# Kernel tuning notes

Hardware: AMD Instinct MI355X
Metric: run time of the kernel (lower is better)

Reference implementation:

```python
import jax, jax.numpy as jnp
import numpy as np

DIM = 768
HEADS = 12
DIM_HEAD = 64
INNER = HEADS * DIM_HEAD  # 768
SCALE = DIM_HEAD ** -0.5
LN_EPS = 1e-5


def setup_inputs() -> dict:
    key = jax.random.key(0)
    ks = jax.random.split(key, 6)
    B, N = 2, 1024
    x = jax.random.normal(ks[0], (B, N, DIM), dtype=jnp.float32)
    ln_g = jnp.ones((DIM,), jnp.float32)
    ln_b = jnp.zeros((DIM,), jnp.float32)
    # torch nn.Linear weights are [out, in]
    w_qkv = jax.random.normal(ks[1], (3 * INNER, DIM), jnp.float32) * (DIM ** -0.5)
    w_out = jax.random.normal(ks[2], (DIM, INNER), jnp.float32) * (INNER ** -0.5)
    b_out = jnp.zeros((DIM,), jnp.float32)
    theta = jax.random.normal(ks[3], (HEADS, HEADS), jnp.float32)
    # xavier_uniform for 12x12
    lim = float(np.sqrt(6.0 / (HEADS + HEADS)))
    gnn_w = jax.random.uniform(ks[4], (HEADS, HEADS), jnp.float32, -lim, lim)
    return {"x": x, "ln_g": ln_g, "ln_b": ln_b, "w_qkv": w_qkv,
            "w_out": w_out, "b_out": b_out, "theta": theta, "gnn_w": gnn_w}


def _dc_crd(attn, theta, gnn_w):
    # attn: [B, H, N, N] treated as image with H=12 channels
    B, H, N, _ = attn.shape
    w = attn.mean(axis=(-2, -1))  # adaptive_avg_pool2d -> [B, H]
    diff = w[:, :, None] - w[:, None, :]  # [B, H, H]
    # abs(1 - exp(-d)/(1+exp(-d))) - 1 == abs(1 - sigmoid(-d)) - 1
    T_w = jnp.abs(1.0 - jax.nn.sigmoid(-diff)) - 1.0
    adj = (T_w + jnp.swapaxes(T_w, -1, -2)) * 0.5 * theta  # [B, H, H]
    attn_flat = attn.reshape(B, H, N * N)
    support = jnp.einsum('ij,bjm->bim', gnn_w, attn_flat)  # W @ features
    out = jax.nn.relu(jnp.einsum('bij,bjm->bim', adj, support))  # spmm(adj, support)
    return out.reshape(B, H, N, N)


def reference(x, ln_g, ln_b, w_qkv, w_out, b_out, theta, gnn_w):
    B, N, D = x.shape
    mu = x.mean(-1, keepdims=True)
    var = x.var(-1, keepdims=True)
    xn = (x - mu) * jax.lax.rsqrt(var + LN_EPS) * ln_g + ln_b
    qkv = xn @ w_qkv.T  # [B, N, 3*INNER]
    q, k, v = jnp.split(qkv, 3, axis=-1)
    def heads(t):
        return t.reshape(B, N, HEADS, DIM_HEAD).transpose(0, 2, 1, 3)
    q, k, v = heads(q), heads(k), heads(v)  # [B, H, N, d]
    dots = jnp.einsum('bhnd,bhmd->bhnm', q, k) * SCALE
    attn = jax.nn.softmax(dots, axis=-1)
    H = _dc_crd(attn, theta, gnn_w)
    out = jnp.einsum('bhnm,bhmd->bhnd', attn + H, v)
    out = out.transpose(0, 2, 1, 3).reshape(B, N, INNER)
    return out @ w_out.T + b_out
```

## Files before the change

kernel.cpp:

```cpp
#include <hip/hip_runtime.h>
#include <hip/hip_bf16.h>
#include <stdint.h>

#define NB 2
#define SEQ 1024
#define DMODEL 768
#define NH 12
#define DH 64
#define SCALE 0.125f
#define NCH 4

#define AJ_RS 1288
#define CT_HS 648

typedef __hip_bfloat16 bf16;
typedef __attribute__((ext_vector_type(8))) short short8;
typedef __attribute__((ext_vector_type(2))) short s2v;
typedef __attribute__((ext_vector_type(4))) float f32x4;

__device__ __forceinline__ bf16 f2b(float x){ return __float2bfloat16(x); }
__device__ __forceinline__ short f2bs(float x){
  bf16 h = __float2bfloat16(x); return *reinterpret_cast<short*>(&h);
}
__device__ __forceinline__ float s2f(short u){
  return __uint_as_float(((unsigned)(unsigned short)u) << 16);
}

__device__ __forceinline__ void gl_lds16(const bf16* g, bf16* l){
  __builtin_amdgcn_global_load_lds(
      (const __attribute__((address_space(1))) void*)g,
      (__attribute__((address_space(3))) void*)l, 16, 0, 0);
}

__global__ __launch_bounds__(256) void prep_all(const float* __restrict__ x,
                                                const float* __restrict__ g,
                                                const float* __restrict__ bta,
                                                const float* __restrict__ w1, int n1,
                                                const float* __restrict__ w2, int n2,
                                                const float* __restrict__ theta,
                                                const float* __restrict__ gnn,
                                                bf16* __restrict__ xn,
                                                bf16* __restrict__ wb,
                                                bf16* __restrict__ Mb,
                                                float* __restrict__ l){
  int bx = blockIdx.x, t = threadIdx.x;
  if (bx < 2048){
    const float* xr = x + (size_t)bx*DMODEL;
    float v0[3]; float s = 0.f, s2 = 0.f;
    #pragma unroll
    for (int i=0;i<3;i++){ float val = xr[t+256*i]; v0[i]=val; s+=val; s2+=val*val; }
    __shared__ float sb[256], s2b[256];
    sb[t]=s; s2b[t]=s2; __syncthreads();
    for (int off=128; off>0; off>>=1){
      if (t<off){ sb[t]+=sb[t+off]; s2b[t]+=s2b[t+off]; }
      __syncthreads();
    }
    float mean = sb[0]*(1.f/DMODEL);
    float var  = s2b[0]*(1.f/DMODEL) - mean*mean;
    float rstd = rsqrtf(var + 1e-5f);
    #pragma unroll
    for (int i=0;i<3;i++){
      int c = t+256*i;
      xn[(size_t)bx*DMODEL + c] = f2b((v0[i]-mean)*rstd*g[c] + bta[c]);
    }
  } else if (bx < 2048+9216){
    int i = (bx-2048)*256 + t;
    if (i < n1) wb[i] = f2b(w1[i]);
    else if (i < n1+n2) wb[i] = f2b(w2[i-n1]);
  } else {
    int sub = bx - (2048+9216);
    if (sub == 0){
      #pragma unroll
      for (int e=0;e<2;e++){
        int idx = t + 256*e;
        int i = idx >> 5, j = idx & 31;
        float sacc = 0.f;
        if (i < 12 && j < 12)
          for (int jj=0;jj<12;jj++) sacc += (-0.5f)*theta[i*12+jj] * gnn[jj*12+j];
        bf16 hi = f2b(sacc);
        float lo = sacc - __bfloat162float(hi);
        Mb[idx]       = hi;
        Mb[512 + idx] = f2b(lo);
      }
    } else {
      l[(sub-1)*256 + t] = 0.f;
    }
  }
}

__global__ __launch_bounds__(256) void gemm_qkv(const bf16* __restrict__ A,
                                                const bf16* __restrict__ W,
                                                bf16* __restrict__ q,
                                                bf16* __restrict__ k,
                                                bf16* __restrict__ vt){
  __shared__ bf16 As[128*32];
  __shared__ bf16 Bs[128*32];
  int n0 = blockIdx.x*128, m0 = blockIdx.y*128;
  int t = threadIdx.x, w = t>>6, lane = t&63;
  int ln16 = lane&15, q8 = (lane>>4)*8;
  int wm = w>>1, wn = w&1;
  f32x4 acc[4][4] = {};
  for (int k0=0; k0<768; k0+=32){
    __syncthreads();
    #pragma unroll
    for (int i=0;i<2;i++){
      int cc = t + i*256;
      int r = cc>>2, ko = (cc&3)*8;
      gl_lds16(&A[(size_t)(m0+r)*768 + k0+ko], &As[(size_t)(w*64 + i*256)*8]);
      gl_lds16(&W[(size_t)(n0+r)*768 + k0+ko], &Bs[(size_t)(w*64 + i*256)*8]);
    }
    __syncthreads();
    short8 af[4], bfr[4];
    #pragma unroll
    for (int mi=0;mi<4;mi++) af[mi]  = *(const short8*)&As[(wm*64+mi*16+ln16)*32 + q8];
    #pragma unroll
    for (int ni=0;ni<4;ni++) bfr[ni] = *(const short8*)&Bs[(wn*64+ni*16+ln16)*32 + q8];
    #pragma unroll
    for (int mi=0;mi<4;mi++)
      #pragma unroll
      for (int ni=0;ni<4;ni++)
        acc[mi][ni] = __builtin_amdgcn_mfma_f32_16x16x32_bf16(af[mi], bfr[ni], acc[mi][ni], 0, 0, 0);
  }
  int quad4 = (lane>>4)*4;
  #pragma unroll
  for (int mi=0;mi<4;mi++){
    #pragma unroll
    for (int ni=0;ni<4;ni++){
      int cg = n0 + wn*64 + ni*16 + ln16;
      int which = cg/768; int rem = cg - which*768;
      int h = rem>>6, dd = rem&63;
      #pragma unroll
      for (int r=0;r<4;r++){
        int m = m0 + wm*64 + mi*16 + quad4 + r;
        int bb = m>>10, n = m&1023;
        float val = acc[mi][ni][r];
        if (which==0)      q [((size_t)(bb*NH+h)*SEQ + n)*DH + dd] = f2b(val*SCALE);
        else if (which==1) k [((size_t)(bb*NH+h)*SEQ + n)*DH + dd] = f2b(val);
        else               vt[((size_t)(bb*NH+h)*DH + dd)*SEQ + n] = f2b(val);
      }
    }
  }
}

__global__ __launch_bounds__(768) void attn_sums(const bf16* __restrict__ q,
                                                 const bf16* __restrict__ k,
                                                 float* __restrict__ l){
  int b = blockIdx.z, ch = blockIdx.y; int r0 = blockIdx.x*16;
  int t = threadIdx.x; int h = t>>6; int lane = t&63;
  int ln16 = lane&15, quad = lane>>4; int q8 = quad*8, quad4 = quad*4;
  const bf16* qrow = q + ((size_t)(b*NH+h)*SEQ + r0 + ln16)*DH;
  short8 aq0 = *(const short8*)(qrow + q8);
  short8 aq1 = *(const short8*)(qrow + 32 + q8);
  const bf16* kB = k + ((size_t)(b*NH+h)*SEQ)*DH;
  float ls[4] = {0.f,0.f,0.f,0.f};
  #pragma unroll 4
  for (int i=0;i<16;i++){
    int c0 = ch*256 + i*16;
    const bf16* krow = kB + (size_t)(c0 + ln16)*DH;
    short8 bk0 = *(const short8*)(krow + q8);
    short8 bk1 = *(const short8*)(krow + 32 + q8);
    f32x4 a = {0.f,0.f,0.f,0.f};
    a = __builtin_amdgcn_mfma_f32_16x16x32_bf16(aq0, bk0, a, 0, 0, 0);
    a = __builtin_amdgcn_mfma_f32_16x16x32_bf16(aq1, bk1, a, 0, 0, 0);
    #pragma unroll
    for (int r=0;r<4;r++) ls[r] += __expf(a[r]);
  }
  #pragma unroll
  for (int msk=1; msk<16; msk<<=1){
    #pragma unroll
    for (int r=0;r<4;r++) ls[r] += __shfl_xor(ls[r], msk);
  }
  if (ln16 == 0){
    #pragma unroll
    for (int r=0;r<4;r++)
      atomicAdd(&l[((size_t)(b*NH+h))*SEQ + r0 + quad4 + r], ls[r]);
  }
}

__global__ __launch_bounds__(768) void attn_main(const bf16* __restrict__ q,
                                                 const bf16* __restrict__ k,
                                                 const bf16* __restrict__ vt,
                                                 const bf16* __restrict__ Mb,
                                                 const float* __restrict__ l,
                                                 bf16* __restrict__ opart){
  __shared__ __align__(16) bf16 attJ[16*AJ_RS];
  __shared__ __align__(16) bf16 combT[16*CT_HS];
  int b = blockIdx.z, ch = blockIdx.y; int r0 = blockIdx.x*16;
  int t = threadIdx.x; int h = t>>6; int lane = t&63;
  int ln16 = lane&15, quad = lane>>4; int q8 = quad*8, quad4 = quad*4;
  const bf16* kB = k  + ((size_t)(b*NH+h)*SEQ)*DH;
  const bf16* vB = vt + ((size_t)(b*NH+h)*DH)*SEQ;

  short8 z8 = (short8){0,0,0,0,0,0,0,0};
  for (int i = t*8; i < 16*AJ_RS; i += 768*8) *(short8*)&attJ[i] = z8;

  short8 mhi = *(const short8*)&Mb[ln16*32 + q8];
  short8 mlo = *(const short8*)&Mb[512 + ln16*32 + q8];

  const bf16* qrow = q + ((size_t)(b*NH+h)*SEQ + r0 + ln16)*DH;
  short8 aq0 = *(const short8*)(qrow + q8);
  short8 aq1 = *(const short8*)(qrow + 32 + q8);

  float inv_l[4];
  #pragma unroll
  for (int r=0;r<4;r++) inv_l[r] = 1.0f / l[((size_t)(b*NH+h))*SEQ + r0 + quad4 + r];

  __syncthreads();

  f32x4 oacc[4] = {};
  for (int it=0; it<8; it++){
    int c0 = ch*256 + it*32;
    #pragma unroll
    for (int half=0; half<2; half++){
      const bf16* krow = kB + (size_t)(c0 + half*16 + ln16)*DH;
      short8 bk0 = *(const short8*)(krow + q8);
      short8 bk1 = *(const short8*)(krow + 32 + q8);
      f32x4 a = {0.f,0.f,0.f,0.f};
      a = __builtin_amdgcn_mfma_f32_16x16x32_bf16(aq0, bk0, a, 0, 0, 0);
      a = __builtin_amdgcn_mfma_f32_16x16x32_bf16(aq1, bk1, a, 0, 0, 0);
      int cc = half*16 + ln16;
      #pragma unroll
      for (int r=0;r<4;r++)
        attJ[(quad4+r)*AJ_RS + cc*40 + h] = f2b(__expf(a[r])*inv_l[r]);
    }
    __syncthreads();
    for (int tl = h; tl < 32; tl += 12){
      int n = tl*16 + ln16;
      int base = (n>>5)*AJ_RS + (n&31)*40;
      short8 bfrag = *(const short8*)&attJ[base + q8];
      f32x4 c = {0.f,0.f,0.f,0.f};
      c = __builtin_amdgcn_mfma_f32_16x16x32_bf16(mlo, bfrag, c, 0, 0, 0);
      c = __builtin_amdgcn_mfma_f32_16x16x32_bf16(mhi, bfrag, c, 0, 0, 0);
      s2v id01 = *(const s2v*)&attJ[base + quad4];
      s2v id23 = *(const s2v*)&attJ[base + quad4 + 2];
      float idf[4] = { s2f(id01[0]), s2f(id01[1]), s2f(id23[0]), s2f(id23[1]) };
      int cbase = (n>>5)*40 + (n&31);
      #pragma unroll
      for (int ri=0; ri<4; ri++)
        combT[(quad4+ri)*CT_HS + cbase] = f2b(idf[ri] + fmaxf(c[ri], 0.f));
    }
    __syncthreads();
    short8 afrag = *(const short8*)&combT[h*CT_HS + ln16*40 + q8];
    #pragma unroll
    for (int ni=0; ni<4; ni++){
      short8 bv = *(const short8*)&vB[(size_t)(ni*16 + ln16)*SEQ + c0 + q8];
      oacc[ni] = __builtin_amdgcn_mfma_f32_16x16x32_bf16(afrag, bv, oacc[ni], 0, 0, 0);
    }
  }
  bf16* dst = opart + ((size_t)ch*NB*SEQ + (size_t)b*SEQ)*DMODEL;
  #pragma unroll
  for (int ni=0; ni<4; ni++)
    #pragma unroll
    for (int r=0; r<4; r++){
      int n = r0 + quad4 + r;
      dst[(size_t)n*DMODEL + h*DH + ni*16 + ln16] = f2b(oacc[ni][r]);
    }
}

__global__ __launch_bounds__(256) void reduce_kernel(const bf16* __restrict__ opart,
                                                     bf16* __restrict__ aout){
  const size_t TOT = (size_t)NB*SEQ*DMODEL;
  size_t i = ((size_t)blockIdx.x*256 + threadIdx.x)*8;
  float s[8] = {};
  #pragma unroll
  for (int c=0;c<NCH;c++){
    short8 u = *(const short8*)&opart[c*TOT + i];
    #pragma unroll
    for (int e=0;e<8;e++) s[e] += s2f(u[e]);
  }
  short8 o;
  #pragma unroll
  for (int e=0;e<8;e++) o[e] = f2bs(s[e]);
  *(short8*)&aout[i] = o;
}

__global__ __launch_bounds__(256) void gemm_out(const bf16* __restrict__ A,
                                                const bf16* __restrict__ W,
                                                const float* __restrict__ bias,
                                                float* __restrict__ out){
  __shared__ bf16 As[64*32];
  __shared__ bf16 Bs[64*32];
  int n0 = blockIdx.x*64, m0 = blockIdx.y*64;
  int t = threadIdx.x, w = t>>6, lane = t&63;
  int ln16 = lane&15, q8 = (lane>>4)*8;
  int wm = w>>1, wn = w&1;
  f32x4 acc[2][2] = {};
  for (int k0=0; k0<768; k0+=32){
    __syncthreads();
    {
      int r = t>>2, ko = (t&3)*8;
      gl_lds16(&A[(size_t)(m0+r)*768 + k0+ko], &As[(size_t)(w*64)*8]);
      gl_lds16(&W[(size_t)(n0+r)*768 + k0+ko], &Bs[(size_t)(w*64)*8]);
    }
    __syncthreads();
    short8 af[2], bfr[2];
    #pragma unroll
    for (int mi=0;mi<2;mi++) af[mi]  = *(const short8*)&As[(wm*32+mi*16+ln16)*32 + q8];
    #pragma unroll
    for (int ni=0;ni<2;ni++) bfr[ni] = *(const short8*)&Bs[(wn*32+ni*16+ln16)*32 + q8];
    #pragma unroll
    for (int mi=0;mi<2;mi++)
      #pragma unroll
      for (int ni=0;ni<2;ni++)
        acc[mi][ni] = __builtin_amdgcn_mfma_f32_16x16x32_bf16(af[mi], bfr[ni], acc[mi][ni], 0, 0, 0);
  }
  int quad4 = (lane>>4)*4;
  #pragma unroll
  for (int mi=0;mi<2;mi++)
    #pragma unroll
    for (int ni=0;ni<2;ni++){
      int cg = n0 + wn*32 + ni*16 + ln16;
      #pragma unroll
      for (int r=0;r<4;r++){
        int m = m0 + wm*32 + mi*16 + quad4 + r;
        out[(size_t)m*768 + cg] = acc[mi][ni][r] + bias[cg];
      }
    }
}

extern "C" void kernel_launch(void* const* d_in, const int* in_sizes, int n_in,
                              void* d_out, int out_size, void* d_ws, size_t ws_size,
                              hipStream_t stream){
  const float* x     = (const float*)d_in[0];
  const float* ln_g  = (const float*)d_in[1];
  const float* ln_b  = (const float*)d_in[2];
  const float* w_qkv = (const float*)d_in[3];
  const float* w_out = (const float*)d_in[4];
  const float* b_out = (const float*)d_in[5];
  const float* theta = (const float*)d_in[6];
  const float* gnn   = (const float*)d_in[7];
  float* out = (float*)d_out;

  char* p = (char*)d_ws;
  bf16* xnb   = (bf16*)p; p += (size_t)2048*768*2;
  bf16* wqkvb = (bf16*)p; p += (size_t)2304*768*2;
  bf16* woutb = (bf16*)p; p += (size_t)768*768*2;
  bf16* qb    = (bf16*)p; p += (size_t)NB*NH*SEQ*DH*2;
  bf16* kb    = (bf16*)p; p += (size_t)NB*NH*SEQ*DH*2;
  bf16* vtb   = (bf16*)p; p += (size_t)NB*NH*SEQ*DH*2;
  bf16* aoutb = (bf16*)p; p += (size_t)2048*768*2;
  bf16* Mbw   = (bf16*)p; p += (size_t)1024*2;
  float* lsum = (float*)p; p += (size_t)NB*NH*SEQ*4;
  bf16* opart = (bf16*)p;

  const int N1 = 2304*768, N2 = 768*768;
  prep_all<<<dim3(2048+9216+97), dim3(256), 0, stream>>>(
      x, ln_g, ln_b, w_qkv, N1, w_out, N2, theta, gnn, xnb, wqkvb, Mbw, lsum);
  gemm_qkv<<<dim3(18, 16), dim3(256), 0, stream>>>(xnb, wqkvb, qb, kb, vtb);
  attn_sums<<<dim3(64, NCH, NB), dim3(768), 0, stream>>>(qb, kb, lsum);
  attn_main<<<dim3(64, NCH, NB), dim3(768), 0, stream>>>(qb, kb, vtb, Mbw, lsum, opart);
  reduce_kernel<<<dim3(NB*SEQ*DMODEL/(8*256)), dim3(256), 0, stream>>>(opart, aoutb);
  gemm_out<<<dim3(12, 32), dim3(256), 0, stream>>>(aoutb, woutb, b_out, out);
}
```

Measured before the change: 202.0 us.

## Fuse partial-sum reduce into out GEMM, prefetch K/V, shrink QKV GEMM tiles

The separate reduce kernel is removed. gemm_out now sums the NCH bf16 partial outputs while staging its A tile into LDS, which drops one launch and one intermediate round trip through global memory. attn_main software-prefetches the next K tile and issues V loads earlier, and gets a minimum-blocks launch bound to help hide load latency. gemm_qkv moves from 128x128 to 64x64 tiles, giving four times as many blocks for better CU coverage, at the cost of less data reuse per block and more register pressure in attn_main.

```diff
diff --git a/kernel.cpp b/kernel.cpp
--- a/kernel.cpp
+++ b/kernel.cpp
@@ -93,47 +93,43 @@
                                                 bf16* __restrict__ q,
                                                 bf16* __restrict__ k,
                                                 bf16* __restrict__ vt){
-  __shared__ bf16 As[128*32];
-  __shared__ bf16 Bs[128*32];
-  int n0 = blockIdx.x*128, m0 = blockIdx.y*128;
+  __shared__ bf16 As[64*32];
+  __shared__ bf16 Bs[64*32];
+  int n0 = blockIdx.x*64, m0 = blockIdx.y*64;
   int t = threadIdx.x, w = t>>6, lane = t&63;
   int ln16 = lane&15, q8 = (lane>>4)*8;
   int wm = w>>1, wn = w&1;
-  f32x4 acc[4][4] = {};
+  f32x4 acc[2][2] = {};
+  int r = t>>2, ko = (t&3)*8;
   for (int k0=0; k0<768; k0+=32){
     __syncthreads();
-    #pragma unroll
-    for (int i=0;i<2;i++){
-      int cc = t + i*256;
-      int r = cc>>2, ko = (cc&3)*8;
-      gl_lds16(&A[(size_t)(m0+r)*768 + k0+ko], &As[(size_t)(w*64 + i*256)*8]);
-      gl_lds16(&W[(size_t)(n0+r)*768 + k0+ko], &Bs[(size_t)(w*64 + i*256)*8]);
-    }
-    __syncthreads();
-    short8 af[4], bfr[4];
-    #pragma unroll
-    for (int mi=0;mi<4;mi++) af[mi]  = *(const short8*)&As[(wm*64+mi*16+ln16)*32 + q8];
-    #pragma unroll
-    for (int ni=0;ni<4;ni++) bfr[ni] = *(const short8*)&Bs[(wn*64+ni*16+ln16)*32 + q8];
-    #pragma unroll
-    for (int mi=0;mi<4;mi++)
-      #pragma unroll
-      for (int ni=0;ni<4;ni++)
+    gl_lds16(&A[(size_t)(m0+r)*768 + k0+ko], &As[(size_t)(w*64)*8]);
+    gl_lds16(&W[(size_t)(n0+r)*768 + k0+ko], &Bs[(size_t)(w*64)*8]);
+    __syncthreads();
+    short8 af[2], bfr[2];
+    #pragma unroll
+    for (int mi=0;mi<2;mi++) af[mi]  = *(const short8*)&As[(wm*32+mi*16+ln16)*32 + q8];
+    #pragma unroll
+    for (int ni=0;ni<2;ni++) bfr[ni] = *(const short8*)&Bs[(wn*32+ni*16+ln16)*32 + q8];
+    #pragma unroll
+    for (int mi=0;mi<2;mi++)
+      #pragma unroll
+      for (int ni=0;ni<2;ni++)
         acc[mi][ni] = __builtin_amdgcn_mfma_f32_16x16x32_bf16(af[mi], bfr[ni], acc[mi][ni], 0, 0, 0);
   }
   int quad4 = (lane>>4)*4;
   #pragma unroll
-  for (int mi=0;mi<4;mi++){
-    #pragma unroll
-    for (int ni=0;ni<4;ni++){
-      int cg = n0 + wn*64 + ni*16 + ln16;
+  for (int mi=0;mi<2;mi++){
+    #pragma unroll
+    for (int ni=0;ni<2;ni++){
+      int cg = n0 + wn*32 + ni*16 + ln16;
       int which = cg/768; int rem = cg - which*768;
       int h = rem>>6, dd = rem&63;
       #pragma unroll
-      for (int r=0;r<4;r++){
-        int m = m0 + wm*64 + mi*16 + quad4 + r;
+      for (int rr=0;rr<4;rr++){
+        int m = m0 + wm*32 + mi*16 + quad4 + rr;
         int bb = m>>10, n = m&1023;
-        float val = acc[mi][ni][r];
+        float val = acc[mi][ni][rr];
         if (which==0)      q [((size_t)(bb*NH+h)*SEQ + n)*DH + dd] = f2b(val*SCALE);
         else if (which==1) k [((size_t)(bb*NH+h)*SEQ + n)*DH + dd] = f2b(val);
         else               vt[((size_t)(bb*NH+h)*DH + dd)*SEQ + n] = f2b(val);
@@ -177,12 +173,12 @@
   }
 }
 
-__global__ __launch_bounds__(768) void attn_main(const bf16* __restrict__ q,
-                                                 const bf16* __restrict__ k,
-                                                 const bf16* __restrict__ vt,
-                                                 const bf16* __restrict__ Mb,
-                                                 const float* __restrict__ l,
-                                                 bf16* __restrict__ opart){
+__global__ __launch_bounds__(768, 6) void attn_main(const bf16* __restrict__ q,
+                                                    const bf16* __restrict__ k,
+                                                    const bf16* __restrict__ vt,
+                                                    const bf16* __restrict__ Mb,
+                                                    const float* __restrict__ l,
+                                                    bf16* __restrict__ opart){
   __shared__ __align__(16) bf16 attJ[16*AJ_RS];
   __shared__ __align__(16) bf16 combT[16*CT_HS];
   int b = blockIdx.z, ch = blockIdx.y; int r0 = blockIdx.x*16;
@@ -205,23 +201,42 @@
   #pragma unroll
   for (int r=0;r<4;r++) inv_l[r] = 1.0f / l[((size_t)(b*NH+h))*SEQ + r0 + quad4 + r];
 
+  const bf16* kr0 = kB + (size_t)(ch*256 + ln16)*DH;
+  short8 ka0 = *(const short8*)(kr0 + q8);
+  short8 ka1 = *(const short8*)(kr0 + 32 + q8);
+  short8 kb0 = *(const short8*)(kr0 + 16*DH + q8);
+  short8 kb1 = *(const short8*)(kr0 + 16*DH + 32 + q8);
+
   __syncthreads();
 
   f32x4 oacc[4] = {};
+  #pragma unroll 2
   for (int it=0; it<8; it++){
     int c0 = ch*256 + it*32;
-    #pragma unroll
-    for (int half=0; half<2; half++){
-      const bf16* krow = kB + (size_t)(c0 + half*16 + ln16)*DH;
-      short8 bk0 = *(const short8*)(krow + q8);
-      short8 bk1 = *(const short8*)(krow + 32 + q8);
+    int cn = ch*256 + ((it+1)&7)*32;
+    const bf16* vp = vB + (size_t)ln16*SEQ + c0 + q8;
+    short8 vv0 = *(const short8*)(vp);
+    short8 vv1 = *(const short8*)(vp + 16*SEQ);
+    const bf16* krn = kB + (size_t)(cn + ln16)*DH;
+    short8 na0 = *(const short8*)(krn + q8);
+    short8 na1 = *(const short8*)(krn + 32 + q8);
+    short8 nb0 = *(const short8*)(krn + 16*DH + q8);
+    short8 nb1 = *(const short8*)(krn + 16*DH + 32 + q8);
+    {
       f32x4 a = {0.f,0.f,0.f,0.f};
-      a = __builtin_amdgcn_mfma_f32_16x16x32_bf16(aq0, bk0, a, 0, 0, 0);
-      a = __builtin_amdgcn_mfma_f32_16x16x32_bf16(aq1, bk1, a, 0, 0, 0);
-      int cc = half*16 + ln16;
+      a = __builtin_amdgcn_mfma_f32_16x16x32_bf16(aq0, ka0, a, 0, 0, 0);
+      a = __builtin_amdgcn_mfma_f32_16x16x32_bf16(aq1, ka1, a, 0, 0, 0);
       #pragma unroll
       for (int r=0;r<4;r++)
-        attJ[(quad4+r)*AJ_RS + cc*40 + h] = f2b(__expf(a[r])*inv_l[r]);
+        attJ[(quad4+r)*AJ_RS + ln16*40 + h] = f2b(__expf(a[r])*inv_l[r]);
+    }
+    {
+      f32x4 a = {0.f,0.f,0.f,0.f};
+      a = __builtin_amdgcn_mfma_f32_16x16x32_bf16(aq0, kb0, a, 0, 0, 0);
+      a = __builtin_amdgcn_mfma_f32_16x16x32_bf16(aq1, kb1, a, 0, 0, 0);
+      #pragma unroll
+      for (int r=0;r<4;r++)
+        attJ[(quad4+r)*AJ_RS + (16+ln16)*40 + h] = f2b(__expf(a[r])*inv_l[r]);
     }
     __syncthreads();
     for (int tl = h; tl < 32; tl += 12){
@@ -240,12 +255,14 @@
         combT[(quad4+ri)*CT_HS + cbase] = f2b(idf[ri] + fmaxf(c[ri], 0.f));
     }
     __syncthreads();
+    short8 vv2 = *(const short8*)(vp + 32*SEQ);
+    short8 vv3 = *(const short8*)(vp + 48*SEQ);
     short8 afrag = *(const short8*)&combT[h*CT_HS + ln16*40 + q8];
-    #pragma unroll
-    for (int ni=0; ni<4; ni++){
-      short8 bv = *(const short8*)&vB[(size_t)(ni*16 + ln16)*SEQ + c0 + q8];
-      oacc[ni] = __builtin_amdgcn_mfma_f32_16x16x32_bf16(afrag, bv, oacc[ni], 0, 0, 0);
-    }
+    oacc[0] = __builtin_amdgcn_mfma_f32_16x16x32_bf16(afrag, vv0, oacc[0], 0, 0, 0);
+    oacc[1] = __builtin_amdgcn_mfma_f32_16x16x32_bf16(afrag, vv1, oacc[1], 0, 0, 0);
+    oacc[2] = __builtin_amdgcn_mfma_f32_16x16x32_bf16(afrag, vv2, oacc[2], 0, 0, 0);
+    oacc[3] = __builtin_amdgcn_mfma_f32_16x16x32_bf16(afrag, vv3, oacc[3], 0, 0, 0);
+    ka0 = na0; ka1 = na1; kb0 = nb0; kb1 = nb1;
   }
   bf16* dst = opart + ((size_t)ch*NB*SEQ + (size_t)b*SEQ)*DMODEL;
   #pragma unroll
@@ -257,41 +274,33 @@
     }
 }
 
-__global__ __launch_bounds__(256) void reduce_kernel(const bf16* __restrict__ opart,
-                                                     bf16* __restrict__ aout){
-  const size_t TOT = (size_t)NB*SEQ*DMODEL;
-  size_t i = ((size_t)blockIdx.x*256 + threadIdx.x)*8;
-  float s[8] = {};
-  #pragma unroll
-  for (int c=0;c<NCH;c++){
-    short8 u = *(const short8*)&opart[c*TOT + i];
-    #pragma unroll
-    for (int e=0;e<8;e++) s[e] += s2f(u[e]);
-  }
-  short8 o;
-  #pragma unroll
-  for (int e=0;e<8;e++) o[e] = f2bs(s[e]);
-  *(short8*)&aout[i] = o;
-}
-
-__global__ __launch_bounds__(256) void gemm_out(const bf16* __restrict__ A,
+__global__ __launch_bounds__(256) void gemm_out(const bf16* __restrict__ opart,
                                                 const bf16* __restrict__ W,
                                                 const float* __restrict__ bias,
                                                 float* __restrict__ out){
   __shared__ bf16 As[64*32];
   __shared__ bf16 Bs[64*32];
+  const size_t TOT = (size_t)NB*SEQ*DMODEL;
   int n0 = blockIdx.x*64, m0 = blockIdx.y*64;
   int t = threadIdx.x, w = t>>6, lane = t&63;
   int ln16 = lane&15, q8 = (lane>>4)*8;
   int wm = w>>1, wn = w&1;
   f32x4 acc[2][2] = {};
+  int r = t>>2, ko = (t&3)*8;
   for (int k0=0; k0<768; k0+=32){
     __syncthreads();
-    {
-      int r = t>>2, ko = (t&3)*8;
-      gl_lds16(&A[(size_t)(m0+r)*768 + k0+ko], &As[(size_t)(w*64)*8]);
-      gl_lds16(&W[(size_t)(n0+r)*768 + k0+ko], &Bs[(size_t)(w*64)*8]);
-    }
+    gl_lds16(&W[(size_t)(n0+r)*768 + k0+ko], &Bs[(size_t)(w*64)*8]);
+    float s[8] = {};
+    #pragma unroll
+    for (int c=0;c<NCH;c++){
+      short8 u = *(const short8*)&opart[(size_t)c*TOT + (size_t)(m0+r)*768 + k0+ko];
+      #pragma unroll
+      for (int e=0;e<8;e++) s[e] += s2f(u[e]);
+    }
+    short8 o8;
+    #pragma unroll
+    for (int e=0;e<8;e++) o8[e] = f2bs(s[e]);
+    *(short8*)&As[r*32 + ko] = o8;
     __syncthreads();
     short8 af[2], bfr[2];
     #pragma unroll
@@ -311,9 +320,9 @@
     for (int ni=0;ni<2;ni++){
       int cg = n0 + wn*32 + ni*16 + ln16;
       #pragma unroll
-      for (int r=0;r<4;r++){
-        int m = m0 + wm*32 + mi*16 + quad4 + r;
-        out[(size_t)m*768 + cg] = acc[mi][ni][r] + bias[cg];
+      for (int rr=0;rr<4;rr++){
+        int m = m0 + wm*32 + mi*16 + quad4 + rr;
+        out[(size_t)m*768 + cg] = acc[mi][ni][rr] + bias[cg];
       }
     }
 }
@@ -338,7 +347,6 @@
   bf16* qb    = (bf16*)p; p += (size_t)NB*NH*SEQ*DH*2;
   bf16* kb    = (bf16*)p; p += (size_t)NB*NH*SEQ*DH*2;
   bf16* vtb   = (bf16*)p; p += (size_t)NB*NH*SEQ*DH*2;
-  bf16* aoutb = (bf16*)p; p += (size_t)2048*768*2;
   bf16* Mbw   = (bf16*)p; p += (size_t)1024*2;
   float* lsum = (float*)p; p += (size_t)NB*NH*SEQ*4;
   bf16* opart = (bf16*)p;
@@ -346,9 +354,8 @@
   const int N1 = 2304*768, N2 = 768*768;
   prep_all<<<dim3(2048+9216+97), dim3(256), 0, stream>>>(
       x, ln_g, ln_b, w_qkv, N1, w_out, N2, theta, gnn, xnb, wqkvb, Mbw, lsum);
-  gemm_qkv<<<dim3(18, 16), dim3(256), 0, stream>>>(xnb, wqkvb, qb, kb, vtb);
+  gemm_qkv<<<dim3(36, 32), dim3(256), 0, stream>>>(xnb, wqkvb, qb, kb, vtb);
   attn_sums<<<dim3(64, NCH, NB), dim3(768), 0, stream>>>(qb, kb, lsum);
   attn_main<<<dim3(64, NCH, NB), dim3(768), 0, stream>>>(qb, kb, vtb, Mbw, lsum, opart);
-  reduce_kernel<<<dim3(NB*SEQ*DMODEL/(8*256)), dim3(256), 0, stream>>>(opart, aoutb);
-  gemm_out<<<dim3(12, 32), dim3(256), 0, stream>>>(aoutb, woutb, b_out, out);
-}
+  gemm_out<<<dim3(12, 32), dim3(256), 0, stream>>>(opart, woutb, b_out, out);
+}
```

Result: slower. 255.1 us (+26.3%).
